# Optimization experiments

Measured on AMD Instinct MI355X. Metric: run time of the kernel, lower is better.

## Reference

```python
import jax, jax.numpy as jnp
import numpy as np
import math

B, W, N = 48, 100, 1000
EMB, H, QKV, LOCAL = 128, 8, 16, 100
L = LOCAL + 1  # depot + local_size neighbors


def pos_enc(length):
    # sinusoidal positional encoding, emb_dim even so no pad needed
    nts = EMB // 2
    inv = jnp.exp(jnp.arange(nts, dtype=jnp.float32) * (-math.log(10000.0) / max(nts - 1, 1)))
    pos = jnp.arange(length, dtype=jnp.float32)
    st = pos[:, None] * inv[None, :]
    return jnp.concatenate([jnp.sin(st), jnp.cos(st)], axis=1)  # [length, EMB]


def setup_inputs() -> dict:
    key = jax.random.key(0)
    ks = jax.random.split(key, 11)
    return {
        "theta": jax.random.uniform(ks[0], (B, W, N), dtype=jnp.float32),
        "dist": jax.random.uniform(ks[1], (B, W, N), dtype=jnp.float32),
        "xy": jax.random.uniform(ks[2], (B, W, N, 2), dtype=jnp.float32),
        "norm_demand": jax.random.uniform(ks[3], (B, W, N), dtype=jnp.float32),
        "ninf_mask": jnp.zeros((B, W, N), jnp.float32),
        "init_w": jax.random.normal(ks[4], (3, EMB), dtype=jnp.float32) * 0.1,
        "init_b": jnp.zeros((EMB,), jnp.float32),
        "cur_token": jax.random.uniform(ks[5], (EMB,), minval=-1.0, maxval=1.0, dtype=jnp.float32),
        "Wq": jax.random.normal(ks[6], (EMB, H * QKV), dtype=jnp.float32) * 0.05,
        "Wk": jax.random.normal(ks[7], (EMB, H * QKV), dtype=jnp.float32) * 0.05,
        "Wv": jax.random.normal(ks[8], (EMB, H * QKV), dtype=jnp.float32) * 0.05,
        "Wc_w": jax.random.normal(ks[9], (H * QKV, EMB), dtype=jnp.float32) * 0.05,
        "Wc_b": jnp.zeros((EMB,), jnp.float32),
    }


def reference(theta, dist, xy, norm_demand, ninf_mask, init_w, init_b, cur_token, Wq, Wk, Wv, Wc_w, Wc_b):
    # depot always masked: dist -= mask => depot distance -> +inf
    mask = ninf_mask.at[:, :, 0].set(-jnp.inf)
    dist_eff = dist - mask  # [B,W,N]

    # k smallest distances among non-depot nodes (topk largest=False)
    neg_vals, idx0 = jax.lax.top_k(-dist_eff[:, :, 1:], LOCAL)
    dvals = -neg_vals
    dvals = jnp.where(jnp.isinf(dvals), 0.0, dvals)
    norm_on = (jnp.max(dvals, axis=-1) != 0.0)[..., None]          # [B,W,1]
    norm_fac = jnp.max(dvals, axis=-1, keepdims=True) + 1e-6       # [B,W,1]

    depot = jnp.zeros((B, W, 1), idx0.dtype)
    idx = jnp.concatenate([depot, idx0 + 1], axis=-1)              # [B,W,L]

    g = lambda a: jnp.take_along_axis(a, idx, axis=-1)
    sd = g(dist_eff)
    sdem = g(norm_demand)
    sm = g(ninf_mask)
    sx = g(xy[..., 0])
    sy = g(xy[..., 1])

    # zero out inf entries (the masked depot slot)
    infm = jnp.isinf(sd)
    sdem = jnp.where(infm, 0.0, sdem)
    sx = jnp.where(infm, 0.0, sx)
    sy = jnp.where(infm, 0.0, sy)

    # per-(b,w) coordinate normalization by max local distance
    sx = jnp.where(norm_on, sx / norm_fac, sx)
    sy = jnp.where(norm_on, sy / norm_fac, sy)

    # euclidean + demand => 3 input features
    sorted_input = jnp.stack([sx, sy, sdem], axis=-1)              # [B,W,L,3]
    init_k = sorted_input @ init_w + init_b + pos_enc(L)[None, None]  # [B,W,L,EMB]

    # cur_token is identical for every (b,w) -> shared query per head
    q = (cur_token @ Wq).reshape(H, QKV)
    k = (init_k @ Wk).reshape(B, W, L, H, QKV)
    v = (init_k @ Wv).reshape(B, W, L, H, QKV)

    score = jnp.einsum('hd,bwlhd->bwhl', q, k) / float(np.sqrt(QKV)) + sm[:, :, None, :]
    attn = jax.nn.softmax(score, axis=-1)
    out = jnp.einsum('bwhl,bwlhd->bwhd', attn, v).reshape(B, W, H * QKV)

    mh = out @ Wc_w + Wc_b                                         # [B,W,EMB]
    score2 = jnp.einsum('bwe,bwle->bwl', mh, init_k) / float(np.sqrt(EMB))

    bi = jnp.arange(B)[:, None, None]
    wi = jnp.arange(W)[None, :, None]
    return jnp.zeros((B, W, N), score2.dtype).at[bi, wi, idx].set(score2)
```

## Files before the change

### kernel.cpp

```cpp
#include <hip/hip_runtime.h>
#include <math.h>

#define Bb   48
#define Ww   100
#define Nn   1000
#define EMB  128
#define Hh   8
#define LL   101
#define LOCALK 100
#define TPB  256
#define PPB  4

typedef _Float16 half2v __attribute__((ext_vector_type(2)));
typedef _Float16 half8v __attribute__((ext_vector_type(8)));

#define WS_A    0
#define WS_PE   1024
#define WS_AC   13952
#define WS_WVI  13984
#define WS_PEA  14496
#define WS_PEH  15304
#define WS_PVH  21768
#define WS_WCT  28424

#define AR_SIZE 6528
#define AR_SEL  4096
#define AR_F3   4512
#define AR_SMK  5728
#define AR_MHH  6144
#define AR_COEF 6400
#define AR_CM   6496

#define WSYNC() do { __builtin_amdgcn_wave_barrier(); asm volatile("" ::: "memory"); } while (0)

__device__ __forceinline__ unsigned f2key(float x) {
    unsigned u = __float_as_uint(x);
    return (u & 0x80000000u) ? ~u : (u | 0x80000000u);
}
__device__ __forceinline__ float key2f(unsigned k) {
    unsigned u = (k & 0x80000000u) ? (k & 0x7fffffffu) : ~k;
    return __uint_as_float(u);
}
__device__ __forceinline__ void dot8(float& c0, float& c1, float& c2, float& c3,
                                     half8v p, half8v a) {
    c0 = __builtin_amdgcn_fdot2(__builtin_shufflevector(p, p, 0, 1),
                                __builtin_shufflevector(a, a, 0, 1), c0, false);
    c1 = __builtin_amdgcn_fdot2(__builtin_shufflevector(p, p, 2, 3),
                                __builtin_shufflevector(a, a, 2, 3), c1, false);
    c2 = __builtin_amdgcn_fdot2(__builtin_shufflevector(p, p, 4, 5),
                                __builtin_shufflevector(a, a, 4, 5), c2, false);
    c3 = __builtin_amdgcn_fdot2(__builtin_shufflevector(p, p, 6, 7),
                                __builtin_shufflevector(a, a, 6, 7), c3, false);
}

__global__ void setup1(const float* __restrict__ cur, const float* __restrict__ Wq,
                       const float* __restrict__ Wk, const float* __restrict__ iw,
                       const float* __restrict__ ib, const float* __restrict__ Wv,
                       float* __restrict__ ws) {
    const int t = threadIdx.x, b = blockIdx.x;
    if (b == 0) {
        __shared__ float qs[EMB];
        __shared__ float as_[Hh * EMB];
        if (t < EMB) {
            float acc = 0.f;
            for (int e = 0; e < EMB; ++e) acc += cur[e] * Wq[e * EMB + t];
            qs[t] = acc;
        }
        __syncthreads();
        for (int i = t; i < Hh * EMB; i += TPB) {
            int h = i >> 7, e = i & 127;
            float acc = 0.f;
            for (int d = 0; d < 16; ++d) acc += Wk[e * EMB + h * 16 + d] * qs[h * 16 + d];
            acc *= 0.25f;
            as_[i] = acc; ws[WS_A + i] = acc;
        }
        __syncthreads();
        if (t < 32) {
            int i = t >> 3, h = t & 7;
            const float* src = (i == 0) ? iw : (i == 1) ? iw + EMB : (i == 2) ? iw + 2 * EMB : ib;
            float acc = 0.f;
            for (int e = 0; e < EMB; ++e) acc += src[e] * as_[h * EMB + e];
            ws[WS_AC + t] = acc;
        }
    } else {
        int base = (b - 1) * TPB + t;
        const float kneg = -0.14619587891040738f;
        if (base < LL * EMB) {
            int l = base >> 7, c = base & 127, ic = c & 63;
            float inv = expf((float)ic * kneg);
            float v = (float)l * inv;
            float r = (c < 64) ? sinf(v) : cosf(v);
            ws[WS_PE + base] = r;
            ((_Float16*)(ws + WS_PEH))[base] = (_Float16)r;
        } else if (base < LL * EMB + 512) {
            int j = base - LL * EMB;
            int iv = j >> 7, hd = j & 127;
            const float* src = (iv == 0) ? iw : (iv == 1) ? iw + EMB : (iv == 2) ? iw + 2 * EMB : ib;
            float acc = 0.f;
            for (int e = 0; e < EMB; ++e) acc += src[e] * Wv[e * EMB + hd];
            ws[WS_WVI + j] = acc;
        }
    }
}

__global__ void setup2a(const float* __restrict__ Wv, float* __restrict__ ws) {
    int idx = blockIdx.x * TPB + threadIdx.x;
    if (idx < 128 * 104) {
        int hd = idx / 104, l = idx - hd * 104;
        float acc = 0.f;
        if (l < LL) {
            const float* pr = ws + WS_PE + l * EMB;
            for (int e = 0; e < EMB; ++e) acc += pr[e] * Wv[e * EMB + hd];
        }
        ((_Float16*)(ws + WS_PVH))[idx] = (_Float16)acc;
    } else if (idx < 128 * 104 + Hh * LL) {
        int j = idx - 128 * 104;
        int h = j / LL, l = j - h * LL;
        const float* pr = ws + WS_PE + l * EMB;
        const float* ar = ws + WS_A + h * EMB;
        float acc = 0.f;
        for (int e = 0; e < EMB; ++e) acc += pr[e] * ar[e];
        ws[WS_PEA + j] = acc;
    }
}

__global__ void setup2b(const float* __restrict__ Wcw, float* __restrict__ ws) {
    int idx = blockIdx.x * TPB + threadIdx.x;
    if (idx < 128 * 128) {
        int e = idx >> 7, hd = idx & 127;
        ((_Float16*)(ws + WS_WCT))[idx] = (_Float16)Wcw[hd * EMB + e];
    }
}

__global__ __launch_bounds__(TPB, 6) void main_kernel(
    const float* __restrict__ dist,
    const float* __restrict__ xy,
    const float* __restrict__ ndem,
    const float* __restrict__ ninf,
    const float* __restrict__ iw,
    const float* __restrict__ ib,
    const float* __restrict__ Wcb,
    const float* __restrict__ ws,
    float* __restrict__ out) {

    __shared__ __align__(16) char smem[PPB][AR_SIZE];
    const int tid  = threadIdx.x;
    const int w    = tid >> 6;
    const int lane = tid & 63;
    const int bw   = blockIdx.x * PPB + w;

    char* A = smem[w];
    int*                hist  = (int*)A;
    unsigned long long* list  = (unsigned long long*)(A + 1024);
    _Float16*           attnh = (_Float16*)A;
    _Float16*           uhh   = (_Float16*)(A + 1792);
    float*              row   = (float*)A;
    int*                sel   = (int*)(A + AR_SEL);
    float*              feat3 = (float*)(A + AR_F3);
    float*              smk   = (float*)(A + AR_SMK);
    _Float16*           mhh   = (_Float16*)(A + AR_MHH);
    float*              coef  = (float*)(A + AR_COEF);
    float*              coefM = (float*)(A + AR_CM);

    const float* distRow = dist + (size_t)bw * Nn;
    const float* maskRow = ninf + (size_t)bw * Nn;

    unsigned long long rk[16];
    #pragma unroll
    for (int r = 0; r < 16; ++r) {
        int i = r * 64 + lane;
        unsigned long long kv = ~0ull;
        if (i >= 1 && i < Nn) {
            float de = distRow[i] - maskRow[i];
            kv = ((unsigned long long)f2key(de) << 32) | (unsigned)i;
        }
        rk[r] = kv;
    }
    ((int4*)hist)[lane] = make_int4(0, 0, 0, 0);
    WSYNC();

    unsigned long long prefix = 0;
    int shift = 56;
    int remRank = 99;
    const unsigned long long ltm = (1ull << lane) - 1ull;
    for (int round = 0; round < 8; ++round) {
        shift = 56 - 8 * round;
        #pragma unroll
        for (int r = 0; r < 16; ++r) {
            unsigned long long kv = rk[r];
            bool in = (kv != ~0ull) &&
                      (round == 0 || (kv >> (shift + 8)) == (prefix >> (shift + 8)));
            if (in) atomicAdd(&hist[(unsigned)((kv >> shift) & 0xffull)], 1);
        }
        WSYNC();
        int4 hv = ((int4*)hist)[lane];
        ((int4*)hist)[lane] = make_int4(0, 0, 0, 0);
        int s = hv.x + hv.y + hv.z + hv.w;
        int incl = s;
        #pragma unroll
        for (int o = 1; o < 64; o <<= 1) { int t = __shfl_up(incl, o, 64); if (lane >= o) incl += t; }
        int e0 = incl - s;
        int e1 = e0 + hv.x, e2 = e1 + hv.y, e3 = e2 + hv.z;
        int bc = -1, ec = 0, cc = 0;
        if (hv.x > 0 && remRank >= e0 && remRank < e1)        { bc = 4*lane+0; ec = e0; cc = hv.x; }
        if (hv.y > 0 && remRank >= e1 && remRank < e2)        { bc = 4*lane+1; ec = e1; cc = hv.y; }
        if (hv.z > 0 && remRank >= e2 && remRank < e3)        { bc = 4*lane+2; ec = e2; cc = hv.z; }
        if (hv.w > 0 && remRank >= e3 && remRank < e3+hv.w)   { bc = 4*lane+3; ec = e3; cc = hv.w; }
        unsigned long long fm = __ballot(bc >= 0);
        int srcl = __ffsll((unsigned long long)fm) - 1;
        bc = __shfl(bc, srcl, 64); ec = __shfl(ec, srcl, 64); cc = __shfl(cc, srcl, 64);
        prefix |= ((unsigned long long)(unsigned)bc) << shift;
        remRank -= ec;
        if (cc == 1) break;
    }

    unsigned long long pk = 0; bool pf = false;
    #pragma unroll
    for (int r = 0; r < 16; ++r)
        if ((rk[r] >> shift) == (prefix >> shift)) { pk = rk[r]; pf = true; }
    {
        unsigned long long fm = __ballot(pf);
        int srcl = __ffsll((unsigned long long)fm) - 1;
        pk = __shfl(pk, srcl, 64);
    }
    const unsigned long long pivot = pk;

    int cnt_run = 0;
    #pragma unroll
    for (int r = 0; r < 16; ++r) {
        bool p = rk[r] <= pivot;
        unsigned long long m = __ballot(p);
        if (p) list[cnt_run + (int)__popcll(m & ltm)] = rk[r];
        cnt_run += (int)__popcll(m);
    }
    WSYNC();

    unsigned long long kv0 = list[lane];
    const bool has1 = lane < (LOCALK - 64);
    unsigned long long kv1 = has1 ? list[lane + 64] : ~0ull;
    int r0 = 0, r1 = 0;
    #pragma unroll 4
    for (int j = 0; j < LOCALK; ++j) {
        unsigned long long lv = list[j];
        r0 += (lv < kv0);
        r1 += (lv < kv1);
    }
    float v0 = key2f((unsigned)(kv0 >> 32));
    bool i0 = isinf(v0);
    sel[r0 + 1] = (int)(kv0 & 0xffffffu) | (i0 ? 0x40000000 : 0);
    float dvm = i0 ? 0.f : v0;
    if (has1) {
        float v1 = key2f((unsigned)(kv1 >> 32));
        bool i1 = isinf(v1);
        sel[r1 + 1] = (int)(kv1 & 0xffffffu) | (i1 ? 0x40000000 : 0);
        dvm = fmaxf(dvm, i1 ? 0.f : v1);
    }
    #pragma unroll
    for (int o = 32; o > 0; o >>= 1) dvm = fmaxf(dvm, __shfl_xor(dvm, o, 64));
    if (lane == 0) sel[0] = 0x40000000;
    const float nmax = dvm;
    const bool  norm_on = (nmax != 0.f);
    const float nfac = nmax + 1e-6f;
    WSYNC();

    auto gather1 = [&](int t) {
        int s = sel[t];
        int n = s & 0xffffff;
        bool infm = (s & 0x40000000) != 0;
        float fx = 0.f, fy = 0.f, fd = 0.f;
        if (!infm) {
            size_t base = (size_t)bw * Nn + n;
            fx = xy[2 * base]; fy = xy[2 * base + 1]; fd = ndem[base];
        }
        if (norm_on) { fx /= nfac; fy /= nfac; }
        feat3[t] = fx; feat3[LL + t] = fy; feat3[2 * LL + t] = fd;
        smk[t] = maskRow[n];
    };
    gather1(lane);
    if (lane < LL - 64) gather1(lane + 64);
    WSYNC();

    const int h = lane >> 3, ln8 = lane & 7;
    {
        const float A0 = ws[WS_AC + h], A1 = ws[WS_AC + 8 + h];
        const float A2 = ws[WS_AC + 16 + h], Cc = ws[WS_AC + 24 + h];
        const float* pea = ws + WS_PEA + h * LL;
        float ev[14];
        float mx = -INFINITY;
        #pragma unroll
        for (int k = 0; k < 14; ++k) {
            int l = ln8 + 8 * k;
            float sv = -INFINITY;
            if (l < LL)
                sv = feat3[l] * A0 + feat3[LL + l] * A1 + feat3[2 * LL + l] * A2
                   + Cc + pea[l] + smk[l];
            ev[k] = sv;
            mx = fmaxf(mx, sv);
        }
        #pragma unroll
        for (int o = 1; o < 8; o <<= 1) mx = fmaxf(mx, __shfl_xor(mx, o, 64));
        float sm = 0.f;
        #pragma unroll
        for (int k = 0; k < 14; ++k) {
            int l = ln8 + 8 * k;
            float e = (l < LL) ? __expf(ev[k] - mx) : 0.f;
            ev[k] = e; sm += e;
        }
        #pragma unroll
        for (int o = 1; o < 8; o <<= 1) sm += __shfl_xor(sm, o, 64);
        const float ainv = 1.f / sm;
        #pragma unroll
        for (int k = 0; k < 14; ++k) {
            int l = ln8 + 8 * k;
            attnh[h * 112 + l] = (_Float16)(ev[k] * ainv);
        }
        float c0 = 0.f, c1 = 0.f, c2 = 0.f;
        #pragma unroll
        for (int k = 0; k < 13; ++k) {
            int l = ln8 + 8 * k;
            if (l < LL) {
                float at = ev[k] * ainv;
                c0 += at * feat3[l]; c1 += at * feat3[LL + l]; c2 += at * feat3[2 * LL + l];
            }
        }
        #pragma unroll
        for (int o = 1; o < 8; o <<= 1) {
            c0 += __shfl_xor(c0, o, 64); c1 += __shfl_xor(c1, o, 64); c2 += __shfl_xor(c2, o, 64);
        }
        if (ln8 == 0) { coef[h * 3 + 0] = c0; coef[h * 3 + 1] = c1; coef[h * 3 + 2] = c2; }
    }
    WSYNC();

    #pragma unroll
    for (int t = 0; t < 2; ++t) {
        int hd = lane + 64 * t;
        int hh = hd >> 4;
        const half8v* pv = (const half8v*)((const _Float16*)(ws + WS_PVH) + hd * 104);
        const half8v* at = (const half8v*)(attnh + hh * 112);
        float d0 = 0.f, d1 = 0.f, d2 = 0.f, d3 = 0.f;
        #pragma unroll
        for (int j = 0; j < 13; ++j) dot8(d0, d1, d2, d3, pv[j], at[j]);
        float u = (d0 + d1) + (d2 + d3)
                + coef[hh * 3 + 0] * ws[WS_WVI + hd]
                + coef[hh * 3 + 1] * ws[WS_WVI + 128 + hd]
                + coef[hh * 3 + 2] * ws[WS_WVI + 256 + hd]
                + ws[WS_WVI + 384 + hd];
        uhh[hd] = (_Float16)u;
    }
    WSYNC();

    #pragma unroll
    for (int t = 0; t < 2; ++t) {
        int e = lane + 64 * t;
        const half8v* wr = (const half8v*)((const _Float16*)(ws + WS_WCT) + e * 128);
        const half8v* ur = (const half8v*)uhh;
        float d0 = 0.f, d1 = 0.f, d2 = 0.f, d3 = 0.f;
        #pragma unroll
        for (int j = 0; j < 16; ++j) dot8(d0, d1, d2, d3, wr[j], ur[j]);
        mhh[e] = (_Float16)(Wcb[e] + (d0 + d1) + (d2 + d3));
    }
    WSYNC();

    {
        int g = lane & 3;
        const float* src = (g == 0) ? iw : (g == 1) ? iw + EMB : (g == 2) ? iw + 2 * EMB : ib;
        float v = 0.f;
        #pragma unroll
        for (int j = 0; j < 8; ++j) {
            int e = (lane >> 2) + 16 * j;
            v += (float)mhh[e] * src[e];
        }
        v += __shfl_xor(v, 4, 64); v += __shfl_xor(v, 8, 64);
        v += __shfl_xor(v, 16, 64); v += __shfl_xor(v, 32, 64);
        if (lane < 4) coefM[lane] = v;
    }
    {
        float4 z = make_float4(0.f, 0.f, 0.f, 0.f);
        ((float4*)row)[lane] = z;
        ((float4*)row)[lane + 64] = z;
        ((float4*)row)[lane + 128] = z;
        if (lane < 58) ((float4*)row)[lane + 192] = z;
    }
    WSYNC();

    auto score2 = [&](int t) {
        float base = feat3[t] * coefM[0] + feat3[LL + t] * coefM[1]
                   + feat3[2 * LL + t] * coefM[2] + coefM[3];
        const half8v* pr = (const half8v*)((const _Float16*)(ws + WS_PEH) + t * 128);
        const half8v* mr = (const half8v*)mhh;
        float d0 = 0.f, d1 = 0.f, d2 = 0.f, d3 = 0.f;
        #pragma unroll
        for (int j = 0; j < 16; ++j) dot8(d0, d1, d2, d3, pr[j], mr[j]);
        row[sel[t] & 0xffffff] = (base + (d0 + d1) + (d2 + d3)) * 0.08838834764831845f;
    };
    score2(lane);
    if (lane < LL - 64) score2(lane + 64);
    WSYNC();

    float* outRow = out + (size_t)bw * Nn;
    ((float4*)outRow)[lane]       = ((float4*)row)[lane];
    ((float4*)outRow)[lane + 64]  = ((float4*)row)[lane + 64];
    ((float4*)outRow)[lane + 128] = ((float4*)row)[lane + 128];
    if (lane < 58) ((float4*)outRow)[lane + 192] = ((float4*)row)[lane + 192];
}

extern "C" void kernel_launch(void* const* d_in, const int* in_sizes, int n_in,
                              void* d_out, int out_size, void* d_ws, size_t ws_size,
                              hipStream_t stream) {
    const float* dist  = (const float*)d_in[1];
    const float* xy    = (const float*)d_in[2];
    const float* ndem  = (const float*)d_in[3];
    const float* ninf  = (const float*)d_in[4];
    const float* initw = (const float*)d_in[5];
    const float* initb = (const float*)d_in[6];
    const float* cur   = (const float*)d_in[7];
    const float* Wq    = (const float*)d_in[8];
    const float* Wk    = (const float*)d_in[9];
    const float* Wv    = (const float*)d_in[10];
    const float* Wcw   = (const float*)d_in[11];
    const float* Wcb   = (const float*)d_in[12];
    float* out = (float*)d_out;
    float* ws  = (float*)d_ws;

    hipLaunchKernelGGL(setup1,  dim3(56), dim3(TPB), 0, stream, cur, Wq, Wk, initw, initb, Wv, ws);
    hipLaunchKernelGGL(setup2a, dim3(56), dim3(TPB), 0, stream, Wv, ws);
    hipLaunchKernelGGL(setup2b, dim3(64), dim3(TPB), 0, stream, Wcw, ws);
    hipLaunchKernelGGL(main_kernel, dim3(Bb * Ww / PPB), dim3(TPB), 0, stream,
                       dist, xy, ndem, ninf, initw, initb, Wcb, ws, out);
}
```

Baseline: 101.9 us.

## Vectorize row loads, replicate radix histograms, and stream-gather features in registers

```diff
diff --git a/kernel.cpp b/kernel.cpp
--- a/kernel.cpp
+++ b/kernel.cpp
@@ -8,8 +8,8 @@
 #define Hh   8
 #define LL   101
 #define LOCALK 100
-#define TPB  256
-#define PPB  4
+#define TPB  128
+#define PPB  2
 
 typedef _Float16 half2v __attribute__((ext_vector_type(2)));
 typedef _Float16 half8v __attribute__((ext_vector_type(8)));
@@ -23,13 +23,7 @@
 #define WS_PVH  21768
 #define WS_WCT  28424
 
-#define AR_SIZE 6528
-#define AR_SEL  4096
-#define AR_F3   4512
-#define AR_SMK  5728
-#define AR_MHH  6144
-#define AR_COEF 6400
-#define AR_CM   6496
+#define AR_SIZE 7584
 
 #define WSYNC() do { __builtin_amdgcn_wave_barrier(); asm volatile("" ::: "memory"); } while (0)
 
@@ -67,7 +61,7 @@
             qs[t] = acc;
         }
         __syncthreads();
-        for (int i = t; i < Hh * EMB; i += TPB) {
+        for (int i = t; i < Hh * EMB; i += 256) {
             int h = i >> 7, e = i & 127;
             float acc = 0.f;
             for (int d = 0; d < 16; ++d) acc += Wk[e * EMB + h * 16 + d] * qs[h * 16 + d];
@@ -83,7 +77,7 @@
             ws[WS_AC + t] = acc;
         }
     } else {
-        int base = (b - 1) * TPB + t;
+        int base = (b - 1) * 256 + t;
         const float kneg = -0.14619587891040738f;
         if (base < LL * EMB) {
             int l = base >> 7, c = base & 127, ic = c & 63;
@@ -104,7 +98,7 @@
 }
 
 __global__ void setup2a(const float* __restrict__ Wv, float* __restrict__ ws) {
-    int idx = blockIdx.x * TPB + threadIdx.x;
+    int idx = blockIdx.x * 256 + threadIdx.x;
     if (idx < 128 * 104) {
         int hd = idx / 104, l = idx - hd * 104;
         float acc = 0.f;
@@ -125,14 +119,14 @@
 }
 
 __global__ void setup2b(const float* __restrict__ Wcw, float* __restrict__ ws) {
-    int idx = blockIdx.x * TPB + threadIdx.x;
+    int idx = blockIdx.x * 256 + threadIdx.x;
     if (idx < 128 * 128) {
         int e = idx >> 7, hd = idx & 127;
         ((_Float16*)(ws + WS_WCT))[idx] = (_Float16)Wcw[hd * EMB + e];
     }
 }
 
-__global__ __launch_bounds__(TPB, 6) void main_kernel(
+__global__ __launch_bounds__(TPB, 5) void main_kernel(
     const float* __restrict__ dist,
     const float* __restrict__ xy,
     const float* __restrict__ ndem,
@@ -150,39 +144,67 @@
     const int bw   = blockIdx.x * PPB + w;
 
     char* A = smem[w];
-    int*                hist  = (int*)A;
-    unsigned long long* list  = (unsigned long long*)(A + 1024);
+    int*                hist4 = (int*)A;
     _Float16*           attnh = (_Float16*)A;
     _Float16*           uhh   = (_Float16*)(A + 1792);
     float*              row   = (float*)A;
-    int*                sel   = (int*)(A + AR_SEL);
-    float*              feat3 = (float*)(A + AR_F3);
-    float*              smk   = (float*)(A + AR_SMK);
-    _Float16*           mhh   = (_Float16*)(A + AR_MHH);
-    float*              coef  = (float*)(A + AR_COEF);
-    float*              coefM = (float*)(A + AR_CM);
+    unsigned long long* list  = (unsigned long long*)(A + 4288);
+    int*                sel   = (int*)(A + 5088);
+    unsigned char*      perm  = (unsigned char*)(A + 5492);
+    float*              smk   = (float*)(A + 5592);
+    float*              feat3 = (float*)(A + 5996);
+    _Float16*           mhh   = (_Float16*)(A + 7216);
+    float*              coef  = (float*)(A + 7472);
+    float*              coefM = (float*)(A + 7568);
 
     const float* distRow = dist + (size_t)bw * Nn;
     const float* maskRow = ninf + (size_t)bw * Nn;
-
+    const float* xyRow   = xy   + (size_t)bw * Nn * 2;
+    const float* demRow  = ndem + (size_t)bw * Nn;
+
+    float dvf[16], mkf[16];
+    {
+        float4 dv[4], mv[4];
+        #pragma unroll
+        for (int c = 0; c < 4; ++c) {
+            int n0 = c * 256 + lane * 4;
+            if (n0 < Nn) {
+                dv[c] = *(const float4*)(distRow + n0);
+                mv[c] = *(const float4*)(maskRow + n0);
+            } else {
+                dv[c] = make_float4(0.f, 0.f, 0.f, 0.f);
+                mv[c] = make_float4(0.f, 0.f, 0.f, 0.f);
+            }
+        }
+        #pragma unroll
+        for (int k = 0; k < 5; ++k) {
+            int idx = lane + 64 * k;
+            if (idx < 260) ((int4*)hist4)[idx] = make_int4(0, 0, 0, 0);
+        }
+        #pragma unroll
+        for (int c = 0; c < 4; ++c) {
+            dvf[4*c+0] = dv[c].x; dvf[4*c+1] = dv[c].y; dvf[4*c+2] = dv[c].z; dvf[4*c+3] = dv[c].w;
+            mkf[4*c+0] = mv[c].x; mkf[4*c+1] = mv[c].y; mkf[4*c+2] = mv[c].z; mkf[4*c+3] = mv[c].w;
+        }
+    }
     unsigned long long rk[16];
     #pragma unroll
     for (int r = 0; r < 16; ++r) {
-        int i = r * 64 + lane;
+        int n = (r >> 2) * 256 + lane * 4 + (r & 3);
         unsigned long long kv = ~0ull;
-        if (i >= 1 && i < Nn) {
-            float de = distRow[i] - maskRow[i];
-            kv = ((unsigned long long)f2key(de) << 32) | (unsigned)i;
+        if (n >= 1 && n < Nn) {
+            float de = dvf[r] - mkf[r];
+            kv = ((unsigned long long)f2key(de) << 32) | (unsigned)n;
         }
         rk[r] = kv;
     }
-    ((int4*)hist)[lane] = make_int4(0, 0, 0, 0);
     WSYNC();
 
     unsigned long long prefix = 0;
     int shift = 56;
     int remRank = 99;
     const unsigned long long ltm = (1ull << lane) - 1ull;
+    const int g0 = (lane >> 4) * 260;
     for (int round = 0; round < 8; ++round) {
         shift = 56 - 8 * round;
         #pragma unroll
@@ -190,22 +212,33 @@
             unsigned long long kv = rk[r];
             bool in = (kv != ~0ull) &&
                       (round == 0 || (kv >> (shift + 8)) == (prefix >> (shift + 8)));
-            if (in) atomicAdd(&hist[(unsigned)((kv >> shift) & 0xffull)], 1);
+            if (in) atomicAdd(&hist4[g0 + (int)((kv >> shift) & 0xffull)], 1);
         }
         WSYNC();
-        int4 hv = ((int4*)hist)[lane];
-        ((int4*)hist)[lane] = make_int4(0, 0, 0, 0);
-        int s = hv.x + hv.y + hv.z + hv.w;
+        int4 h0 = *(int4*)&hist4[0 * 260 + 4 * lane];
+        int4 h1 = *(int4*)&hist4[1 * 260 + 4 * lane];
+        int4 h2 = *(int4*)&hist4[2 * 260 + 4 * lane];
+        int4 h3 = *(int4*)&hist4[3 * 260 + 4 * lane];
+        int4 z = make_int4(0, 0, 0, 0);
+        *(int4*)&hist4[0 * 260 + 4 * lane] = z;
+        *(int4*)&hist4[1 * 260 + 4 * lane] = z;
+        *(int4*)&hist4[2 * 260 + 4 * lane] = z;
+        *(int4*)&hist4[3 * 260 + 4 * lane] = z;
+        int cx = h0.x + h1.x + h2.x + h3.x;
+        int cy = h0.y + h1.y + h2.y + h3.y;
+        int cz = h0.z + h1.z + h2.z + h3.z;
+        int cw = h0.w + h1.w + h2.w + h3.w;
+        int s = cx + cy + cz + cw;
         int incl = s;
         #pragma unroll
         for (int o = 1; o < 64; o <<= 1) { int t = __shfl_up(incl, o, 64); if (lane >= o) incl += t; }
         int e0 = incl - s;
-        int e1 = e0 + hv.x, e2 = e1 + hv.y, e3 = e2 + hv.z;
+        int e1 = e0 + cx, e2 = e1 + cy, e3 = e2 + cz;
         int bc = -1, ec = 0, cc = 0;
-        if (hv.x > 0 && remRank >= e0 && remRank < e1)        { bc = 4*lane+0; ec = e0; cc = hv.x; }
-        if (hv.y > 0 && remRank >= e1 && remRank < e2)        { bc = 4*lane+1; ec = e1; cc = hv.y; }
-        if (hv.z > 0 && remRank >= e2 && remRank < e3)        { bc = 4*lane+2; ec = e2; cc = hv.z; }
-        if (hv.w > 0 && remRank >= e3 && remRank < e3+hv.w)   { bc = 4*lane+3; ec = e3; cc = hv.w; }
+        if (cx > 0 && remRank >= e0 && remRank < e1)      { bc = 4*lane+0; ec = e0; cc = cx; }
+        if (cy > 0 && remRank >= e1 && remRank < e2)      { bc = 4*lane+1; ec = e1; cc = cy; }
+        if (cz > 0 && remRank >= e2 && remRank < e3)      { bc = 4*lane+2; ec = e2; cc = cz; }
+        if (cw > 0 && remRank >= e3 && remRank < e3 + cw) { bc = 4*lane+3; ec = e3; cc = cw; }
         unsigned long long fm = __ballot(bc >= 0);
         int srcl = __ffsll((unsigned long long)fm) - 1;
         bc = __shfl(bc, srcl, 64); ec = __shfl(ec, srcl, 64); cc = __shfl(cc, srcl, 64);
@@ -213,7 +246,6 @@
         remRank -= ec;
         if (cc == 1) break;
     }
-
     unsigned long long pk = 0; bool pf = false;
     #pragma unroll
     for (int r = 0; r < 16; ++r)
@@ -235,49 +267,83 @@
     }
     WSYNC();
 
-    unsigned long long kv0 = list[lane];
-    const bool has1 = lane < (LOCALK - 64);
-    unsigned long long kv1 = has1 ? list[lane + 64] : ~0ull;
-    int r0 = 0, r1 = 0;
-    #pragma unroll 4
-    for (int j = 0; j < LOCALK; ++j) {
-        unsigned long long lv = list[j];
-        r0 += (lv < kv0);
-        r1 += (lv < kv1);
-    }
-    float v0 = key2f((unsigned)(kv0 >> 32));
-    bool i0 = isinf(v0);
-    sel[r0 + 1] = (int)(kv0 & 0xffffffu) | (i0 ? 0x40000000 : 0);
-    float dvm = i0 ? 0.f : v0;
-    if (has1) {
-        float v1 = key2f((unsigned)(kv1 >> 32));
-        bool i1 = isinf(v1);
-        sel[r1 + 1] = (int)(kv1 & 0xffffffu) | (i1 ? 0x40000000 : 0);
-        dvm = fmaxf(dvm, i1 ? 0.f : v1);
-    }
-    #pragma unroll
-    for (int o = 32; o > 0; o >>= 1) dvm = fmaxf(dvm, __shfl_xor(dvm, o, 64));
-    if (lane == 0) sel[0] = 0x40000000;
-    const float nmax = dvm;
-    const bool  norm_on = (nmax != 0.f);
-    const float nfac = nmax + 1e-6f;
-    WSYNC();
-
-    auto gather1 = [&](int t) {
-        int s = sel[t];
-        int n = s & 0xffffff;
-        bool infm = (s & 0x40000000) != 0;
-        float fx = 0.f, fy = 0.f, fd = 0.f;
-        if (!infm) {
-            size_t base = (size_t)bw * Nn + n;
-            fx = xy[2 * base]; fy = xy[2 * base + 1]; fd = ndem[base];
-        }
-        if (norm_on) { fx /= nfac; fy /= nfac; }
-        feat3[t] = fx; feat3[LL + t] = fy; feat3[2 * LL + t] = fd;
-        smk[t] = maskRow[n];
-    };
-    gather1(lane);
-    if (lane < LL - 64) gather1(lane + 64);
+    {
+        unsigned long long kv0 = list[lane];
+        const bool has1 = lane < (LOCALK - 64);
+        unsigned long long kv1 = has1 ? list[lane + 64] : ~0ull;
+        int r0 = 0, r1 = 0;
+        #pragma unroll 4
+        for (int j = 0; j < LOCALK; ++j) {
+            unsigned long long lv = list[j];
+            r0 += (lv < kv0);
+            r1 += (lv < kv1);
+        }
+        float v0 = key2f((unsigned)(kv0 >> 32));
+        float dvm = isinf(v0) ? 0.f : v0;
+        perm[lane] = (unsigned char)(r0 + 1);
+        if (has1) {
+            float v1 = key2f((unsigned)(kv1 >> 32));
+            perm[lane + 64] = (unsigned char)(r1 + 1);
+            dvm = fmaxf(dvm, isinf(v1) ? 0.f : v1);
+        }
+        #pragma unroll
+        for (int o = 32; o > 0; o >>= 1) dvm = fmaxf(dvm, __shfl_xor(dvm, o, 64));
+        const float nmax = dvm;
+        const bool  norm_on = (nmax != 0.f);
+        const float nfac = nmax + 1e-6f;
+        WSYNC();
+
+        int crun = 0;
+        #pragma unroll
+        for (int half = 0; half < 2; ++half) {
+            float xs[8], ys[8], dd[8];
+            #pragma unroll
+            for (int cl = 0; cl < 2; ++cl) {
+                int c = half * 2 + cl;
+                int n0 = c * 256 + lane * 4;
+                float4 a0, a1, d0;
+                if (n0 < Nn) {
+                    a0 = *(const float4*)(xyRow + 2 * n0);
+                    a1 = *(const float4*)(xyRow + 2 * n0 + 4);
+                    d0 = *(const float4*)(demRow + n0);
+                } else {
+                    a0 = a1 = d0 = make_float4(0.f, 0.f, 0.f, 0.f);
+                }
+                xs[4*cl+0] = a0.x; ys[4*cl+0] = a0.y;
+                xs[4*cl+1] = a0.z; ys[4*cl+1] = a0.w;
+                xs[4*cl+2] = a1.x; ys[4*cl+2] = a1.y;
+                xs[4*cl+3] = a1.z; ys[4*cl+3] = a1.w;
+                dd[4*cl+0] = d0.x; dd[4*cl+1] = d0.y; dd[4*cl+2] = d0.z; dd[4*cl+3] = d0.w;
+            }
+            #pragma unroll
+            for (int q = 0; q < 8; ++q) {
+                int r = half * 8 + q;
+                unsigned long long kv = rk[r];
+                bool p = kv <= pivot;
+                unsigned long long m = __ballot(p);
+                int pos = crun + (int)__popcll(m & ltm);
+                crun += (int)__popcll(m);
+                if (p) {
+                    int rnk = perm[pos];
+                    float val = key2f((unsigned)(kv >> 32));
+                    bool infm = isinf(val);
+                    float fx = infm ? 0.f : xs[q];
+                    float fy = infm ? 0.f : ys[q];
+                    float fd = infm ? 0.f : dd[q];
+                    if (norm_on) { fx /= nfac; fy /= nfac; }
+                    int n = (int)(kv & 0xffffffu);
+                    feat3[rnk] = fx; feat3[101 + rnk] = fy; feat3[202 + rnk] = fd;
+                    smk[rnk] = mkf[r];
+                    sel[rnk] = n | (infm ? 0x40000000 : 0);
+                }
+            }
+        }
+        if (lane == 0) {
+            feat3[0] = 0.f; feat3[101] = 0.f; feat3[202] = 0.f;
+            smk[0] = mkf[0];
+            sel[0] = 0x40000000;
+        }
+    }
     WSYNC();
 
     const int h = lane >> 3, ln8 = lane & 7;
@@ -292,7 +358,7 @@
             int l = ln8 + 8 * k;
             float sv = -INFINITY;
             if (l < LL)
-                sv = feat3[l] * A0 + feat3[LL + l] * A1 + feat3[2 * LL + l] * A2
+                sv = feat3[l] * A0 + feat3[101 + l] * A1 + feat3[202 + l] * A2
                    + Cc + pea[l] + smk[l];
             ev[k] = sv;
             mx = fmaxf(mx, sv);
@@ -320,7 +386,7 @@
             int l = ln8 + 8 * k;
             if (l < LL) {
                 float at = ev[k] * ainv;
-                c0 += at * feat3[l]; c1 += at * feat3[LL + l]; c2 += at * feat3[2 * LL + l];
+                c0 += at * feat3[l]; c1 += at * feat3[101 + l]; c2 += at * feat3[202 + l];
             }
         }
         #pragma unroll
@@ -384,8 +450,8 @@
     WSYNC();
 
     auto score2 = [&](int t) {
-        float base = feat3[t] * coefM[0] + feat3[LL + t] * coefM[1]
-                   + feat3[2 * LL + t] * coefM[2] + coefM[3];
+        float base = feat3[t] * coefM[0] + feat3[101 + t] * coefM[1]
+                   + feat3[202 + t] * coefM[2] + coefM[3];
         const half8v* pr = (const half8v*)((const _Float16*)(ws + WS_PEH) + t * 128);
         const half8v* mr = (const half8v*)mhh;
         float d0 = 0.f, d1 = 0.f, d2 = 0.f, d3 = 0.f;
@@ -422,9 +488,9 @@
     float* out = (float*)d_out;
     float* ws  = (float*)d_ws;
 
-    hipLaunchKernelGGL(setup1,  dim3(56), dim3(TPB), 0, stream, cur, Wq, Wk, initw, initb, Wv, ws);
-    hipLaunchKernelGGL(setup2a, dim3(56), dim3(TPB), 0, stream, Wv, ws);
-    hipLaunchKernelGGL(setup2b, dim3(64), dim3(TPB), 0, stream, Wcw, ws);
+    hipLaunchKernelGGL(setup1,  dim3(56), dim3(256), 0, stream, cur, Wq, Wk, initw, initb, Wv, ws);
+    hipLaunchKernelGGL(setup2a, dim3(56), dim3(256), 0, stream, Wv, ws);
+    hipLaunchKernelGGL(setup2b, dim3(64), dim3(256), 0, stream, Wcw, ws);
     hipLaunchKernelGGL(main_kernel, dim3(Bb * Ww / PPB), dim3(TPB), 0, stream,
                        dist, xy, ndem, ninf, initw, initb, Wcb, ws, out);
 }
```

Measured after the change: 101.6 us (median of 2 runs). No clear change (-0.3%).
